# Performance work log

Hardware: AMD Instinct MI355X
Metric: run time of the kernel (lower is better)

Reference implementation:

```python
import jax, jax.numpy as jnp
import numpy as np


def setup_inputs() -> dict:
    key = jax.random.key(0)
    ks = jax.random.split(key, 6)
    B, L, V, D, H, C = 2048, 200, 50000, 300, 32, 3
    x = jax.random.randint(ks[0], (B, L), 0, V)
    lengths = jax.random.randint(ks[1], (B,), 1, L + 1)
    emb_table = jax.random.normal(ks[2], (V, D), dtype=jnp.float32)
    W1 = jax.random.normal(ks[3], (D, H), dtype=jnp.float32) * (1.0 / np.sqrt(D))
    b1 = jnp.zeros((H,), dtype=jnp.float32)
    W2 = jax.random.normal(ks[4], (H, C), dtype=jnp.float32) * (1.0 / np.sqrt(H))
    b2 = jnp.zeros((C,), dtype=jnp.float32)
    return {"x": x, "lengths": lengths, "emb_table": emb_table,
            "W1": W1, "b1": b1, "W2": W2, "b2": b2}


def reference(x, lengths, emb_table, W1, b1, W2, b2):
    # Embedding gather: [B, L, D]
    emb = emb_table[x]
    # Length-normalized sum over the (padded) sequence, matching the torch
    # loop which sums ALL L positions and divides by lengths[i].
    rep = emb.sum(axis=1) / lengths[:, None].astype(emb.dtype)  # [B, D]
    h = jax.nn.relu(rep @ W1 + b1)  # [B, 32]
    logits = h @ W2 + b2            # [B, C]
    return logits
```

## Files before the change

### kernel.cpp

```cpp
#include <hip/hip_runtime.h>
#include <hip/hip_bf16.h>

typedef __attribute__((ext_vector_type(8))) short short8;
typedef __attribute__((ext_vector_type(4))) short short4v;
typedef __attribute__((ext_vector_type(4))) float floatx4;

__device__ float Pbuf[50000 * 32];

__device__ __forceinline__ short tobf16(float f) {
    unsigned u = __builtin_bit_cast(unsigned, f);
    u += 0x7fffu + ((u >> 16) & 1u);
    return (short)(u >> 16);
}

#define APAD 336

__global__ __launch_bounds__(256, 1) void project_kernel(
        const float* __restrict__ E, const float* __restrict__ W1, int V) {
    __shared__ __align__(16) short w1t[32][APAD];
    __shared__ __align__(16) short atile[2][64][APAD];

    int tid   = threadIdx.x;
    int b     = blockIdx.x;
    int tiles = (V + 63) >> 6;
    int NT    = (tiles - b + 255) >> 8;

    for (int idx = tid; idx < 2 * 64 * 20; idx += 256) {
        int bufi = idx / (64 * 20);
        int rem  = idx % (64 * 20);
        atile[bufi][rem / 20][300 + rem % 20] = 0;
    }
    for (int idx = tid; idx < 32 * 20; idx += 256)
        w1t[idx / 20][300 + idx % 20] = 0;

    int arow = tid >> 2;
    int aq   = tid & 3;

    floatx4 wreg[10];
#pragma unroll
    for (int r = 0; r < 10; ++r) {
        int ch = tid + (r << 8);
        if (ch < 2400) wreg[r] = *(const floatx4*)(W1 + (size_t)ch * 4);
    }
    floatx4 areg[19];
    {
        int t0 = b;
        int nrows0 = min(64, V - (t0 << 6));
        const float* eb = E + ((size_t)t0 << 6) * 300;
#pragma unroll
        for (int j = 0; j < 19; ++j) {
            int c = aq + 4 * j;
            if (c < 75 && arow < nrows0)
                areg[j] = *(const floatx4*)(eb + (size_t)arow * 300 + c * 4);
        }
    }
#pragma unroll
    for (int r = 0; r < 10; ++r) {
        int ch = tid + (r << 8);
        if (ch < 2400) {
            int flat = ch * 4;
            int k = flat >> 5, n0 = flat & 31;
#pragma unroll
            for (int jj = 0; jj < 4; ++jj) w1t[n0 + jj][k] = tobf16(wreg[r][jj]);
        }
    }
    {
        int nrows0 = min(64, V - (b << 6));
#pragma unroll
        for (int j = 0; j < 19; ++j) {
            int c = aq + 4 * j;
            if (c < 75 && arow < nrows0) {
                short4v s;
#pragma unroll
                for (int jj = 0; jj < 4; ++jj) s[jj] = tobf16(areg[j][jj]);
                *(short4v*)&atile[0][arow][c * 4] = s;
            }
        }
    }
    __syncthreads();

    int lane = tid & 63;
    int w    = tid >> 6;
    int m    = lane & 15;
    int quad = lane >> 4;
    int rowbase = w << 4;

    for (int i = 0; i < NT; ++i) {
        int t   = b + (i << 8);
        int cur = i & 1;
        bool pf = (i + 1 < NT);
        int tn  = t + 256;
        int nrowsN = pf ? min(64, V - (tn << 6)) : 0;

        const float* eb2 = E + ((size_t)tn << 6) * 300;
#pragma unroll
        for (int j = 0; j < 19; ++j) {
            int c = aq + 4 * j;
            if (pf && c < 75 && arow < nrowsN)
                areg[j] = *(const floatx4*)(eb2 + (size_t)arow * 300 + c * 4);
        }

        int nrows = min(64, V - (t << 6));
        if (rowbase < nrows) {
            floatx4 acc0 = {0.f, 0.f, 0.f, 0.f};
            floatx4 acc1 = {0.f, 0.f, 0.f, 0.f};
#pragma unroll
            for (int s = 0; s < 10; ++s) {
                int kc = s * 32 + quad * 8;
                short8 a  = *(const short8*)&atile[cur][rowbase + m][kc];
                short8 b0 = *(const short8*)&w1t[m][kc];
                short8 b1 = *(const short8*)&w1t[16 + m][kc];
                acc0 = __builtin_amdgcn_mfma_f32_16x16x32_bf16(a, b0, acc0, 0, 0, 0);
                acc1 = __builtin_amdgcn_mfma_f32_16x16x32_bf16(a, b1, acc1, 0, 0, 0);
            }
#pragma unroll
            for (int r = 0; r < 4; ++r) {
                int row = (t << 6) + rowbase + quad * 4 + r;
                Pbuf[(size_t)row * 32 + m]      = acc0[r];
                Pbuf[(size_t)row * 32 + 16 + m] = acc1[r];
            }
        }

        if (pf) {
#pragma unroll
            for (int j = 0; j < 19; ++j) {
                int c = aq + 4 * j;
                if (c < 75 && arow < nrowsN) {
                    short4v s;
#pragma unroll
                    for (int jj = 0; jj < 4; ++jj) s[jj] = tobf16(areg[j][jj]);
                    *(short4v*)&atile[cur ^ 1][arow][c * 4] = s;
                }
            }
        }
        __syncthreads();
    }
}

__global__ __launch_bounds__(256) void pool_mlp_kernel(
        const int* __restrict__ x, const int* __restrict__ lengths,
        const float* __restrict__ b1, const float* __restrict__ W2,
        const float* __restrict__ b2, float* __restrict__ out, int L, int C) {
    __shared__ int   xs[512];
    __shared__ float red[4][32];
    int b    = blockIdx.x;
    int w    = threadIdx.x >> 6;
    int lane = threadIdx.x & 63;
    int h    = lane & 31;
    int th   = lane >> 5;

    const int* xrow = x + (size_t)b * L;
    for (int i = threadIdx.x; i < L; i += 256) xs[i] = xrow[i];
    __syncthreads();

    int Lw    = (L + 3) >> 2;
    int start = w * Lw;
    int end   = min(start + Lw, L);

    float acc = 0.f;
    int t = start;
    for (; t + 8 <= end; t += 8) {
        int i0 = xs[t + th];
        int i1 = xs[t + 2 + th];
        int i2 = xs[t + 4 + th];
        int i3 = xs[t + 6 + th];
        float v0 = Pbuf[(size_t)i0 * 32 + h];
        float v1 = Pbuf[(size_t)i1 * 32 + h];
        float v2 = Pbuf[(size_t)i2 * 32 + h];
        float v3 = Pbuf[(size_t)i3 * 32 + h];
        acc += v0; acc += v1; acc += v2; acc += v3;
    }
    for (; t < end; t += 2) {
        int tt = t + th;
        if (tt < end) acc += Pbuf[(size_t)xs[tt] * 32 + h];
    }
    acc += __shfl_xor(acc, 32, 64);
    if (lane < 32) red[w][h] = acc;
    __syncthreads();

    if (threadIdx.x < 32) {
        float s    = red[0][h] + red[1][h] + red[2][h] + red[3][h];
        float lenf = (float)lengths[b];
        float hv   = fmaxf(s / lenf + b1[h], 0.f);
        for (int c = 0; c < C; ++c) {
            float p = hv * W2[h * C + c];
            p += __shfl_xor(p, 16, 64);
            p += __shfl_xor(p, 8, 64);
            p += __shfl_xor(p, 4, 64);
            p += __shfl_xor(p, 2, 64);
            p += __shfl_xor(p, 1, 64);
            if (threadIdx.x == 0) out[(size_t)b * C + c] = p + b2[c];
        }
    }
}

__global__ void naive_dnn(const int* __restrict__ x, const int* __restrict__ len,
                          const float* __restrict__ emb, const float* __restrict__ W1,
                          const float* __restrict__ b1, const float* __restrict__ W2,
                          const float* __restrict__ b2, float* __restrict__ out,
                          int L, int V, int D, int H, int C) {
    __shared__ float srep[2048];
    __shared__ float sh[256];
    int b = blockIdx.x;
    float lenf = (float)len[b];
    for (int d = threadIdx.x; d < D; d += blockDim.x) {
        float acc = 0.f;
        for (int l = 0; l < L; ++l) {
            int idx = x[(size_t)b * L + l];
            acc += emb[(size_t)idx * D + d];
        }
        srep[d] = acc / lenf;
    }
    __syncthreads();
    for (int hh = threadIdx.x; hh < H; hh += blockDim.x) {
        float a = b1[hh];
        for (int d = 0; d < D; ++d) a += srep[d] * W1[(size_t)d * H + hh];
        sh[hh] = fmaxf(a, 0.f);
    }
    __syncthreads();
    for (int c = threadIdx.x; c < C; c += blockDim.x) {
        float a = b2[c];
        for (int hh = 0; hh < H; ++hh) a += sh[hh] * W2[hh * C + c];
        out[(size_t)b * C + c] = a;
    }
}

extern "C" void kernel_launch(void* const* d_in, const int* in_sizes, int n_in,
                              void* d_out, int out_size, void* d_ws, size_t ws_size,
                              hipStream_t stream) {
    const int*   x       = (const int*)d_in[0];
    const int*   lengths = (const int*)d_in[1];
    const float* emb     = (const float*)d_in[2];
    const float* W1      = (const float*)d_in[3];
    const float* b1      = (const float*)d_in[4];
    const float* W2      = (const float*)d_in[5];
    const float* b2      = (const float*)d_in[6];
    float* out = (float*)d_out;

    int B = in_sizes[1];
    int L = in_sizes[0] / B;
    int H = in_sizes[4];
    int C = in_sizes[6];
    int D = in_sizes[3] / H;
    int V = in_sizes[2] / D;

    bool fast = (D == 300) && (H == 32) && (V == 50000) && (L <= 512);
    if (fast) {
        int tiles  = (V + 63) >> 6;
        int blocks = min(256, tiles);
        project_kernel<<<blocks, 256, 0, stream>>>(emb, W1, V);
        pool_mlp_kernel<<<B, 256, 0, stream>>>(x, lengths, b1, W2, b2, out, L, C);
    } else {
        naive_dnn<<<B, 256, 0, stream>>>(x, lengths, emb, W1, b1, W2, b2, out,
                                         L, V, D, H, C);
    }
}
```

Baseline: 114.8 us.

## Halve projection tile rows, split N across waves, keep W1 fragments in registers

The projection kernel now processes 32-row tiles instead of 64, launches 512 blocks with occupancy hint 2, and splits the 32 output columns across wave pairs so each wave does one MFMA chain. Each wave's W1 B-fragments are loaded once into registers rather than re-read from LDS every tile. Pbuf stores are moved after the next tile's LDS conversion, and a scheduling barrier is added after the prefetch loads. This aims for more concurrent blocks per CU and less LDS traffic, at the cost of more tile iterations and more per-tile sync overhead.

```diff
diff --git a/kernel.cpp b/kernel.cpp
--- a/kernel.cpp
+++ b/kernel.cpp
@@ -15,26 +15,26 @@
 
 #define APAD 336
 
-__global__ __launch_bounds__(256, 1) void project_kernel(
+__global__ __launch_bounds__(256, 2) void project_kernel(
         const float* __restrict__ E, const float* __restrict__ W1, int V) {
     __shared__ __align__(16) short w1t[32][APAD];
-    __shared__ __align__(16) short atile[2][64][APAD];
+    __shared__ __align__(16) short atile[2][32][APAD];
 
     int tid   = threadIdx.x;
     int b     = blockIdx.x;
-    int tiles = (V + 63) >> 6;
-    int NT    = (tiles - b + 255) >> 8;
-
-    for (int idx = tid; idx < 2 * 64 * 20; idx += 256) {
-        int bufi = idx / (64 * 20);
-        int rem  = idx % (64 * 20);
+    int tiles = (V + 31) >> 5;
+    int NT    = (tiles - b + 511) >> 9;
+
+    for (int idx = tid; idx < 2 * 32 * 20; idx += 256) {
+        int bufi = idx / (32 * 20);
+        int rem  = idx % (32 * 20);
         atile[bufi][rem / 20][300 + rem % 20] = 0;
     }
     for (int idx = tid; idx < 32 * 20; idx += 256)
         w1t[idx / 20][300 + idx % 20] = 0;
 
-    int arow = tid >> 2;
-    int aq   = tid & 3;
+    int arow = tid >> 3;
+    int aq   = tid & 7;
 
     floatx4 wreg[10];
 #pragma unroll
@@ -42,14 +42,13 @@
         int ch = tid + (r << 8);
         if (ch < 2400) wreg[r] = *(const floatx4*)(W1 + (size_t)ch * 4);
     }
-    floatx4 areg[19];
+    floatx4 areg[10];
     {
-        int t0 = b;
-        int nrows0 = min(64, V - (t0 << 6));
-        const float* eb = E + ((size_t)t0 << 6) * 300;
-#pragma unroll
-        for (int j = 0; j < 19; ++j) {
-            int c = aq + 4 * j;
+        int nrows0 = min(32, V - (b << 5));
+        const float* eb = E + ((size_t)b << 5) * 300;
+#pragma unroll
+        for (int j = 0; j < 10; ++j) {
+            int c = aq + 8 * j;
             if (c < 75 && arow < nrows0)
                 areg[j] = *(const floatx4*)(eb + (size_t)arow * 300 + c * 4);
         }
@@ -65,10 +64,10 @@
         }
     }
     {
-        int nrows0 = min(64, V - (b << 6));
-#pragma unroll
-        for (int j = 0; j < 19; ++j) {
-            int c = aq + 4 * j;
+        int nrows0 = min(32, V - (b << 5));
+#pragma unroll
+        for (int j = 0; j < 10; ++j) {
+            int c = aq + 8 * j;
             if (c < 75 && arow < nrows0) {
                 short4v s;
 #pragma unroll
@@ -79,52 +78,48 @@
     }
     __syncthreads();
 
-    int lane = tid & 63;
-    int w    = tid >> 6;
-    int m    = lane & 15;
-    int quad = lane >> 4;
-    int rowbase = w << 4;
+    int lane   = tid & 63;
+    int w      = tid >> 6;
+    int m      = lane & 15;
+    int quad   = lane >> 4;
+    int rowsub = (w & 1) << 4;
+    int ncol0  = (w >> 1) << 4;
+
+    short8 bfrag[10];
+#pragma unroll
+    for (int s = 0; s < 10; ++s)
+        bfrag[s] = *(const short8*)&w1t[ncol0 + m][s * 32 + quad * 8];
 
     for (int i = 0; i < NT; ++i) {
-        int t   = b + (i << 8);
+        int t   = b + (i << 9);
         int cur = i & 1;
         bool pf = (i + 1 < NT);
-        int tn  = t + 256;
-        int nrowsN = pf ? min(64, V - (tn << 6)) : 0;
-
-        const float* eb2 = E + ((size_t)tn << 6) * 300;
-#pragma unroll
-        for (int j = 0; j < 19; ++j) {
-            int c = aq + 4 * j;
+        int tn  = t + 512;
+        int nrowsN = pf ? min(32, V - (tn << 5)) : 0;
+
+        const float* eb2 = E + ((size_t)tn << 5) * 300;
+#pragma unroll
+        for (int j = 0; j < 10; ++j) {
+            int c = aq + 8 * j;
             if (pf && c < 75 && arow < nrowsN)
                 areg[j] = *(const floatx4*)(eb2 + (size_t)arow * 300 + c * 4);
         }
-
-        int nrows = min(64, V - (t << 6));
-        if (rowbase < nrows) {
-            floatx4 acc0 = {0.f, 0.f, 0.f, 0.f};
-            floatx4 acc1 = {0.f, 0.f, 0.f, 0.f};
+        __builtin_amdgcn_sched_barrier(0);
+
+        int nrows = min(32, V - (t << 5));
+        floatx4 acc = {0.f, 0.f, 0.f, 0.f};
+        if (rowsub < nrows) {
 #pragma unroll
             for (int s = 0; s < 10; ++s) {
-                int kc = s * 32 + quad * 8;
-                short8 a  = *(const short8*)&atile[cur][rowbase + m][kc];
-                short8 b0 = *(const short8*)&w1t[m][kc];
-                short8 b1 = *(const short8*)&w1t[16 + m][kc];
-                acc0 = __builtin_amdgcn_mfma_f32_16x16x32_bf16(a, b0, acc0, 0, 0, 0);
-                acc1 = __builtin_amdgcn_mfma_f32_16x16x32_bf16(a, b1, acc1, 0, 0, 0);
-            }
-#pragma unroll
-            for (int r = 0; r < 4; ++r) {
-                int row = (t << 6) + rowbase + quad * 4 + r;
-                Pbuf[(size_t)row * 32 + m]      = acc0[r];
-                Pbuf[(size_t)row * 32 + 16 + m] = acc1[r];
+                short8 a = *(const short8*)&atile[cur][rowsub + m][s * 32 + quad * 8];
+                acc = __builtin_amdgcn_mfma_f32_16x16x32_bf16(a, bfrag[s], acc, 0, 0, 0);
             }
         }
 
         if (pf) {
 #pragma unroll
-            for (int j = 0; j < 19; ++j) {
-                int c = aq + 4 * j;
+            for (int j = 0; j < 10; ++j) {
+                int c = aq + 8 * j;
                 if (c < 75 && arow < nrowsN) {
                     short4v s;
 #pragma unroll
@@ -133,6 +128,15 @@
                 }
             }
         }
+
+        if (rowsub < nrows) {
+#pragma unroll
+            for (int r = 0; r < 4; ++r) {
+                int row = (t << 5) + rowsub + quad * 4 + r;
+                Pbuf[(size_t)row * 32 + ncol0 + m] = acc[r];
+            }
+        }
+
         __syncthreads();
     }
 }
@@ -246,8 +250,8 @@
 
     bool fast = (D == 300) && (H == 32) && (V == 50000) && (L <= 512);
     if (fast) {
-        int tiles  = (V + 63) >> 6;
-        int blocks = min(256, tiles);
+        int tiles  = (V + 31) >> 5;
+        int blocks = min(512, tiles);
         project_kernel<<<blocks, 256, 0, stream>>>(emb, W1, V);
         pool_mlp_kernel<<<B, 256, 0, stream>>>(x, lengths, b1, W2, b2, out, L, C);
     } else {
```

Result: no change. 112.7 us (-1.8%).

## Replace persistent double-buffered projection loop with one 16-row tile per wave

Applied to the files above, without the earlier changes.

The projection kernel no longer runs a persistent 256-block grid looping over 64-row tiles with register prefetch and double buffering. It launches about 782 blocks, and each wave loads, converts and multiplies one 16-row tile of the embedding table against W1. The LDS stride is tighter and launch bounds now allow two blocks per CU, so more waves are in flight to hide the memory latency of streaming the table. The cost is that every block reloads and converts W1 into shared memory, and there is no longer any software pipelining inside a block.

```diff
diff --git a/kernel.cpp b/kernel.cpp
--- a/kernel.cpp
+++ b/kernel.cpp
@@ -13,28 +13,19 @@
     return (short)(u >> 16);
 }
 
-#define APAD 336
-
-__global__ __launch_bounds__(256, 1) void project_kernel(
+#define ASTR 312
+__global__ __launch_bounds__(256, 2) void project_kernel(
         const float* __restrict__ E, const float* __restrict__ W1, int V) {
-    __shared__ __align__(16) short w1t[32][APAD];
-    __shared__ __align__(16) short atile[2][64][APAD];
-
-    int tid   = threadIdx.x;
-    int b     = blockIdx.x;
-    int tiles = (V + 63) >> 6;
-    int NT    = (tiles - b + 255) >> 8;
-
-    for (int idx = tid; idx < 2 * 64 * 20; idx += 256) {
-        int bufi = idx / (64 * 20);
-        int rem  = idx % (64 * 20);
-        atile[bufi][rem / 20][300 + rem % 20] = 0;
-    }
-    for (int idx = tid; idx < 32 * 20; idx += 256)
-        w1t[idx / 20][300 + idx % 20] = 0;
-
-    int arow = tid >> 2;
-    int aq   = tid & 3;
+    __shared__ __align__(16) short w1t[32][336];
+    __shared__ __align__(16) short afl[4][5008];
+
+    int tid  = threadIdx.x;
+    int lane = tid & 63;
+    int w    = tid >> 6;
+
+    int tiles = V >> 4;
+    int t     = (blockIdx.x << 2) + w;
+    bool has  = t < tiles;
 
     floatx4 wreg[10];
 #pragma unroll
@@ -42,18 +33,27 @@
         int ch = tid + (r << 8);
         if (ch < 2400) wreg[r] = *(const floatx4*)(W1 + (size_t)ch * 4);
     }
-    floatx4 areg[19];
+    int arow = lane >> 2, aq = lane & 3;
+    const float* ebase = E + ((size_t)t * 16 + arow) * 300;
+    floatx4 ra[19];
+#pragma unroll
+    for (int j = 0; j < 19; ++j) {
+        int c = aq + (j << 2);
+        if (has && c < 75) ra[j] = *(const floatx4*)(ebase + c * 4);
+    }
+    __builtin_amdgcn_sched_barrier(0);
+
+    for (int idx = tid; idx < 32 * 36; idx += 256)
+        w1t[idx / 36][300 + idx % 36] = 0;
     {
-        int t0 = b;
-        int nrows0 = min(64, V - (t0 << 6));
-        const float* eb = E + ((size_t)t0 << 6) * 300;
-#pragma unroll
-        for (int j = 0; j < 19; ++j) {
-            int c = aq + 4 * j;
-            if (c < 75 && arow < nrows0)
-                areg[j] = *(const floatx4*)(eb + (size_t)arow * 300 + c * 4);
-        }
-    }
+        short* as = &afl[w][0];
+        for (int i = lane; i < 208; i += 64) {
+            int idx = (i < 192) ? ((i / 12) * ASTR + 300 + i % 12)
+                                : (16 * ASTR + (i - 192));
+            as[idx] = 0;
+        }
+    }
+
 #pragma unroll
     for (int r = 0; r < 10; ++r) {
         int ch = tid + (r << 8);
@@ -64,76 +64,42 @@
             for (int jj = 0; jj < 4; ++jj) w1t[n0 + jj][k] = tobf16(wreg[r][jj]);
         }
     }
-    {
-        int nrows0 = min(64, V - (b << 6));
+    __syncthreads();
+
+    short* as = &afl[w][0];
+    if (has) {
 #pragma unroll
         for (int j = 0; j < 19; ++j) {
-            int c = aq + 4 * j;
-            if (c < 75 && arow < nrows0) {
-                short4v s;
-#pragma unroll
-                for (int jj = 0; jj < 4; ++jj) s[jj] = tobf16(areg[j][jj]);
-                *(short4v*)&atile[0][arow][c * 4] = s;
+            int c = aq + (j << 2);
+            if (c < 75) {
+                short4v s4;
+#pragma unroll
+                for (int jj = 0; jj < 4; ++jj) s4[jj] = tobf16(ra[j][jj]);
+                *(short4v*)(as + arow * ASTR + c * 4) = s4;
             }
         }
     }
-    __syncthreads();
-
-    int lane = tid & 63;
-    int w    = tid >> 6;
+
     int m    = lane & 15;
     int quad = lane >> 4;
-    int rowbase = w << 4;
-
-    for (int i = 0; i < NT; ++i) {
-        int t   = b + (i << 8);
-        int cur = i & 1;
-        bool pf = (i + 1 < NT);
-        int tn  = t + 256;
-        int nrowsN = pf ? min(64, V - (tn << 6)) : 0;
-
-        const float* eb2 = E + ((size_t)tn << 6) * 300;
-#pragma unroll
-        for (int j = 0; j < 19; ++j) {
-            int c = aq + 4 * j;
-            if (pf && c < 75 && arow < nrowsN)
-                areg[j] = *(const floatx4*)(eb2 + (size_t)arow * 300 + c * 4);
-        }
-
-        int nrows = min(64, V - (t << 6));
-        if (rowbase < nrows) {
-            floatx4 acc0 = {0.f, 0.f, 0.f, 0.f};
-            floatx4 acc1 = {0.f, 0.f, 0.f, 0.f};
-#pragma unroll
-            for (int s = 0; s < 10; ++s) {
-                int kc = s * 32 + quad * 8;
-                short8 a  = *(const short8*)&atile[cur][rowbase + m][kc];
-                short8 b0 = *(const short8*)&w1t[m][kc];
-                short8 b1 = *(const short8*)&w1t[16 + m][kc];
-                acc0 = __builtin_amdgcn_mfma_f32_16x16x32_bf16(a, b0, acc0, 0, 0, 0);
-                acc1 = __builtin_amdgcn_mfma_f32_16x16x32_bf16(a, b1, acc1, 0, 0, 0);
-            }
-#pragma unroll
-            for (int r = 0; r < 4; ++r) {
-                int row = (t << 6) + rowbase + quad * 4 + r;
-                Pbuf[(size_t)row * 32 + m]      = acc0[r];
-                Pbuf[(size_t)row * 32 + 16 + m] = acc1[r];
-            }
-        }
-
-        if (pf) {
-#pragma unroll
-            for (int j = 0; j < 19; ++j) {
-                int c = aq + 4 * j;
-                if (c < 75 && arow < nrowsN) {
-                    short4v s;
-#pragma unroll
-                    for (int jj = 0; jj < 4; ++jj) s[jj] = tobf16(areg[j][jj]);
-                    *(short4v*)&atile[cur ^ 1][arow][c * 4] = s;
-                }
-            }
-        }
-        __syncthreads();
+    if (has) {
+        floatx4 acc0 = {0.f, 0.f, 0.f, 0.f};
+        floatx4 acc1 = {0.f, 0.f, 0.f, 0.f};
+#pragma unroll
+        for (int s = 0; s < 10; ++s) {
+            int kc = s * 32 + quad * 8;
+            short8 a  = *(const short8*)(as + m * ASTR + kc);
+            short8 b0 = *(const short8*)&w1t[m][kc];
+            short8 b1 = *(const short8*)&w1t[16 + m][kc];
+            acc0 = __builtin_amdgcn_mfma_f32_16x16x32_bf16(a, b0, acc0, 0, 0, 0);
+            acc1 = __builtin_amdgcn_mfma_f32_16x16x32_bf16(a, b1, acc1, 0, 0, 0);
+        }
+#pragma unroll
+        for (int r = 0; r < 4; ++r) {
+            int row = (t << 4) + quad * 4 + r;
+            Pbuf[(size_t)row * 32 + m]      = acc0[r];
+            Pbuf[(size_t)row * 32 + 16 + m] = acc1[r];
+        }
     }
 }
 
@@ -246,8 +212,8 @@
 
     bool fast = (D == 300) && (H == 32) && (V == 50000) && (L <= 512);
     if (fast) {
-        int tiles  = (V + 63) >> 6;
-        int blocks = min(256, tiles);
+        int tiles  = V >> 4;
+        int blocks = (tiles + 3) >> 2;
         project_kernel<<<blocks, 256, 0, stream>>>(emb, W1, V);
         pool_mlp_kernel<<<B, 256, 0, stream>>>(x, lengths, b1, W2, b2, out, L, C);
     } else {
```

After: 113.7 us. No clear change (-1.0%).
